# Kernel optimization log

Hardware: AMD Instinct MI355X
Metric: run time of the kernel (lower is better)

The kernel has to match this reference:

```python
import jax, jax.numpy as jnp
import numpy as np

BOX = 256      # box_size
OS = 1         # oversampling
NC = 10        # n_classes
B = 16         # batch
N = 262144     # points per example


def setup_inputs() -> dict:
    key = jax.random.key(0)
    k1, k2 = jax.random.split(key)
    # coordinates in [-0.5, 0.5) so (points+0.5)*S lies inside the grid
    points = jax.random.uniform(k1, (B, 2, N), dtype=jnp.float32, minval=-0.5, maxval=0.5)
    values = jax.random.normal(k2, (B, NC, N), dtype=jnp.float32)
    return {"points": points, "values": values}


def reference(points, values):
    S = BOX * OS
    b, nc = points.shape[0], values.shape[1]
    # [B,2,N] -> [B,N,2], scaled into pixel coords
    p = jnp.swapaxes((points + 0.5) * S, 1, 2)
    xyf = jnp.floor(p)
    r = p - xyf                       # fractional part, [B,N,2]
    xy = xyf.astype(jnp.int32)
    x, y = xy[..., 0], xy[..., 1]     # [B,N]
    rx, ry = r[..., 0], r[..., 1]

    im = jnp.zeros((b, nc, S * S), dtype=values.dtype)

    def scat(acc, idx, contrib):
        # acc [NC, S*S], idx [N], contrib [NC, N]
        return acc.at[:, idx].add(contrib)

    scat_b = jax.vmap(scat)  # over batch

    # 4-corner bilinear (CIC) deposition
    for dx in (0, 1):
        x_ = x + dx
        wx = (1 - dx) + (2 * dx - 1) * rx
        for dy in (0, 1):
            y_ = y + dy
            wy = (1 - dy) + (2 * dy - 1) * ry
            valid = (x_ >= 0) & (x_ < S) & (y_ >= 0) & (y_ < S)
            idx = jnp.where(valid, y_ * S + x_, 0)           # [B,N]
            w = jnp.where(valid, wx * wy, 0.0)               # [B,N]
            im = scat_b(im, idx, w[:, None, :] * values)     # [B,NC,S*S]

    return im.reshape(b, nc, S, S)
```

## Files before the change

### kernel.cpp

```cpp
#include <hip/hip_runtime.h>

#define S_     256
#define NC_    10
#define CHUNK  1024
#define NBIN   256
#define CAPR   1536
#define CAP    1536
#define RSTR   7

typedef unsigned int u32;

__device__ __forceinline__ u32 f2bf(float f) {
    u32 u = __float_as_uint(f);
    return (u + 0x7fffu + ((u >> 16) & 1u)) >> 16;
}
__device__ __forceinline__ float bf2f(u32 h) { return __uint_as_float(h << 16); }


__global__ void __launch_bounds__(256)
k_scatter(const float* __restrict__ points, const float* __restrict__ values,
          u32* __restrict__ cursor, u32* __restrict__ ovfCnt,
          u32* __restrict__ ovfBuf, uint2* __restrict__ recs, int N) {
    __shared__ u32 cnt[NBIN];
    __shared__ u32 gOff[NBIN];
    __shared__ u32 wsum[4];
    __shared__ unsigned char binId[CHUNK];
    __shared__ u32 lw[6][CHUNK];

    const int tid = threadIdx.x;
    const int cpb = N / CHUNK;
    const int b  = blockIdx.x / cpb;
    const int n0 = (blockIdx.x % cpb) * CHUNK;
    const float* pb = points + (size_t)b * 2 * N;
    const float* vb = values + (size_t)b * NC_ * N;
    const int nb = n0 + tid * 4;

    cnt[tid] = 0;

    const float4 pxv = *(const float4*)(pb + nb);
    const float4 pyv = *(const float4*)(pb + (size_t)N + nb);
    float4 vv[NC_];
#pragma unroll
    for (int c = 0; c < NC_; ++c)
        vv[c] = *(const float4*)(vb + (size_t)c * N + nb);

    __syncthreads();

    float px4[4] = {pxv.x, pxv.y, pxv.z, pxv.w};
    float py4[4] = {pyv.x, pyv.y, pyv.z, pyv.w};
    u32 w0[4], binA[4];
#pragma unroll
    for (int k = 0; k < 4; ++k) {
        float px = (px4[k] + 0.5f) * (float)S_;
        float py = (py4[k] + 0.5f) * (float)S_;
        int xi = (int)floorf(px), yi = (int)floorf(py);
        u32 qx = __float2uint_rn((px - (float)(xi & ~15)) * 2048.0f);
        u32 qy = __float2uint_rn((py - (float)(yi & ~15)) * 2048.0f);
        qx = min(qx, 32767u); qy = min(qy, 32767u);
        w0[k] = qx | (qy << 16);
        binA[k] = (u32)(((yi >> 4) << 4) + (xi >> 4));
        atomicAdd(&cnt[binA[k]], 1u);
    }
    __syncthreads();

    u32 myCnt = cnt[tid];
    u32 x = myCnt;
#pragma unroll
    for (int off = 1; off < 64; off <<= 1) {
        u32 y = __shfl_up(x, off, 64);
        if ((tid & 63) >= off) x += y;
    }
    if ((tid & 63) == 63) wsum[tid >> 6] = x;
    __syncthreads();
    u32 add = 0;
#pragma unroll
    for (int w = 0; w < 4; ++w) add += (w < (tid >> 6)) ? wsum[w] : 0;
    u32 excl = x - myCnt + add;

    const u32 gt = (u32)b * NBIN + (u32)tid;
    u32 gbase = 0;
    if (myCnt) gbase = gt * (u32)CAPR + atomicAdd(&cursor[gt], myCnt);
    gOff[tid] = gbase - excl;
    cnt[tid] = excl;
    __syncthreads();

#pragma unroll
    for (int k = 0; k < 4; ++k) {
        u32 bin = binA[k];
        u32 slot = atomicAdd(&cnt[bin], 1u);
        binId[slot] = (unsigned char)bin;
#define VG(c) ((&vv[c].x)[k])
        lw[0][slot] = w0[k];
        lw[1][slot] = f2bf(VG(0)) | (f2bf(VG(1)) << 16);
        lw[2][slot] = f2bf(VG(2)) | (f2bf(VG(3)) << 16);
        lw[3][slot] = f2bf(VG(4)) | (f2bf(VG(5)) << 16);
        lw[4][slot] = f2bf(VG(6)) | (f2bf(VG(7)) << 16);
        lw[5][slot] = f2bf(VG(8)) | (f2bf(VG(9)) << 16);
#undef VG
    }
    __syncthreads();

    const u32 tb0 = (u32)b * NBIN;
#pragma unroll
    for (int k = 0; k < 4; ++k) {
        u32 r = (u32)tid + (u32)k * 256;
        u32 bin = binId[r];
        u32 dst = gOff[bin] + r;
        u32 a0 = lw[0][r], a1 = lw[1][r], a2 = lw[2][r],
            a3 = lw[3][r], a4 = lw[4][r], a5 = lw[5][r];
        u32 rel = dst - (tb0 + bin) * (u32)CAPR;
        if (rel < (u32)CAPR) {
            size_t s3 = (size_t)dst * 3;
            recs[s3]     = make_uint2(a0, a1);
            recs[s3 + 1] = make_uint2(a2, a3);
            recs[s3 + 2] = make_uint2(a4, a5);
        } else {
            u32 oi = atomicAdd(ovfCnt, 1u);
            u32* ob = ovfBuf + (size_t)oi * 7;
            ob[0] = tb0 + bin;
            ob[1] = a0; ob[2] = a1; ob[3] = a2;
            ob[4] = a3; ob[5] = a4; ob[6] = a5;
        }
    }
}

__global__ void __launch_bounds__(256)
k_fused(const uint2* __restrict__ recs, const u32* __restrict__ cursor,
        float* __restrict__ out, float* __restrict__ borderBuf) {
    __shared__ u32 cnt[NBIN];
    __shared__ u32 excl[NBIN];
    __shared__ u32 wsum[4];
    __shared__ u32 lrec[CAP * RSTR];

    const int tid = threadIdx.x;
    const int g = blockIdx.x;
    const int batch = g >> 8, t = g & 255;
    const int ox = (t & 15) * 16, oy = (t >> 4) * 16;
    const u32 base = (u32)g * (u32)CAPR;
    const u32 n = min(cursor[g], (u32)CAP);

    cnt[tid] = 0;
    __syncthreads();

    u32 r[6][6];
    int cell[6];
#pragma unroll
    for (int k = 0; k < 6; ++k) {
        int i = k * 256 + tid;
        cell[k] = -1;
        if (i < (int)n) {
            size_t sa = (size_t)(base + i) * 3;
            uint2 a = recs[sa], b2 = recs[sa + 1], c2 = recs[sa + 2];
            r[k][0] = a.x;  r[k][1] = a.y;
            r[k][2] = b2.x; r[k][3] = b2.y;
            r[k][4] = c2.x; r[k][5] = c2.y;
            u32 qx = a.x & 0xffffu, qy = a.x >> 16;
            cell[k] = (int)(((qy >> 11) << 4) | (qx >> 11));
            atomicAdd(&cnt[cell[k]], 1u);
        }
    }
    __syncthreads();

    u32 c = cnt[tid];
    u32 x = c;
#pragma unroll
    for (int off = 1; off < 64; off <<= 1) {
        u32 y = __shfl_up(x, off, 64);
        if ((tid & 63) >= off) x += y;
    }
    if ((tid & 63) == 63) wsum[tid >> 6] = x;
    __syncthreads();
    u32 add = 0;
#pragma unroll
    for (int w = 0; w < 4; ++w) add += (w < (tid >> 6)) ? wsum[w] : 0;
    u32 ex = x - c + add;
    excl[tid] = ex;
    cnt[tid] = ex;
    __syncthreads();

#pragma unroll
    for (int k = 0; k < 6; ++k) {
        if (cell[k] >= 0) {
            u32 o = atomicAdd(&cnt[cell[k]], 1u) * RSTR;
#pragma unroll
            for (int w = 0; w < 6; ++w) lrec[o + w] = r[k][w];
        }
    }
    __syncthreads();

    for (int p = tid; p < 289; p += 256) {
        int lx = p % 17, ly = p / 17;
        float acc[NC_];
#pragma unroll
        for (int q = 0; q < NC_; ++q) acc[q] = 0.0f;
#pragma unroll
        for (int dy = 0; dy < 2; ++dy) {
            int cy = ly - 1 + dy;
            if ((unsigned)cy >= 16u) continue;
#pragma unroll
            for (int dx = 0; dx < 2; ++dx) {
                int cx = lx - 1 + dx;
                if ((unsigned)cx >= 16u) continue;
                int cc = (cy << 4) | cx;
                u32 j1 = cnt[cc];
                for (u32 j = excl[cc]; j < j1; ++j) {
                    u32 o = j * RSTR;
                    u32 w0 = lrec[o];
                    float rx = (float)(w0 & 2047u)         * (1.0f / 2048.0f);
                    float ry = (float)((w0 >> 16) & 2047u) * (1.0f / 2048.0f);
                    float w = (dx ? (1.0f - rx) : rx) * (dy ? (1.0f - ry) : ry);
                    u32 w1 = lrec[o + 1], w2 = lrec[o + 2], w3 = lrec[o + 3],
                        w4 = lrec[o + 4], w5 = lrec[o + 5];
                    acc[0] += w * bf2f(w1 & 0xffffu); acc[1] += w * bf2f(w1 >> 16);
                    acc[2] += w * bf2f(w2 & 0xffffu); acc[3] += w * bf2f(w2 >> 16);
                    acc[4] += w * bf2f(w3 & 0xffffu); acc[5] += w * bf2f(w3 >> 16);
                    acc[6] += w * bf2f(w4 & 0xffffu); acc[7] += w * bf2f(w4 >> 16);
                    acc[8] += w * bf2f(w5 & 0xffffu); acc[9] += w * bf2f(w5 >> 16);
                }
            }
        }
        bool interior = (lx >= 1) & (lx <= 15) & (ly >= 1) & (ly <= 15);
        if (interior) {
            int gx = ox + lx, gy = oy + ly;
            float* ob = out + (size_t)batch * NC_ * S_ * S_ + gy * S_ + gx;
#pragma unroll
            for (int q = 0; q < NC_; ++q) ob[(size_t)q * S_ * S_] = acc[q];
        } else {
            float* bb = borderBuf + ((size_t)g * 289 + p) * NC_;
#pragma unroll
            for (int q = 0; q < NC_; ++q) bb[q] = acc[q];
        }
    }
}

#define CLEAN_T 4096
__global__ void __launch_bounds__(256)
k_border(const float* __restrict__ borderBuf, float* __restrict__ out,
         const u32* __restrict__ ovfCnt, const u32* __restrict__ ovfBuf,
         int total) {
    int idx = blockIdx.x * 256 + threadIdx.x;
    if (idx >= total) {
        u32 oc = *ovfCnt;
        for (u32 j = (u32)(idx - total); j < oc; j += CLEAN_T) {
            const u32* ob = ovfBuf + (size_t)j * 7;
            u32 g = ob[0];
            int batch = (int)(g >> 8), t = (int)(g & 255u);
            int ox = (t & 15) * 16, oy = (t >> 4) * 16;
            u32 w0 = ob[1];
            u32 qx = w0 & 0xffffu, qy = w0 >> 16;
            int xi = ox + (int)(qx >> 11), yi = oy + (int)(qy >> 11);
            float rx = (float)(qx & 2047u) * (1.0f / 2048.0f);
            float ry = (float)(qy & 2047u) * (1.0f / 2048.0f);
            float v[NC_];
            v[0] = bf2f(ob[2] & 0xffffu); v[1] = bf2f(ob[2] >> 16);
            v[2] = bf2f(ob[3] & 0xffffu); v[3] = bf2f(ob[3] >> 16);
            v[4] = bf2f(ob[4] & 0xffffu); v[5] = bf2f(ob[4] >> 16);
            v[6] = bf2f(ob[5] & 0xffffu); v[7] = bf2f(ob[5] >> 16);
            v[8] = bf2f(ob[6] & 0xffffu); v[9] = bf2f(ob[6] >> 16);
            float* obase = out + (size_t)batch * NC_ * S_ * S_;
            for (int dx = 0; dx < 2; ++dx) {
                int x_ = xi + dx; if (x_ >= S_) continue;
                float wx = dx ? rx : (1.0f - rx);
                for (int dy = 0; dy < 2; ++dy) {
                    int y_ = yi + dy; if (y_ >= S_) continue;
                    float w = wx * (dy ? ry : (1.0f - ry));
                    for (int cc = 0; cc < NC_; ++cc)
                        atomicAdd(obase + (size_t)cc * S_ * S_ + y_ * S_ + x_,
                                  w * v[cc]);
                }
            }
        }
        return;
    }
    int b = idx / 7936;
    int j = idx - b * 7936;
    int gx, gy;
    if (j < 4096) {
        gx = (j >> 8) << 4;
        gy = j & 255;
    } else {
        int j2 = j - 4096;
        int row = j2 / 240, col = j2 - row * 240;
        gy = row << 4;
        gx = col + 1 + col / 15;
    }

    int txs[2], lxs[2], nx = 0;
    bool bx = (gx & 15) == 0, by = (gy & 15) == 0;
    if (bx) {
        if (gx > 0) { txs[nx] = (gx >> 4) - 1; lxs[nx] = 16; ++nx; }
        txs[nx] = gx >> 4; lxs[nx] = 0; ++nx;
    } else { txs[0] = gx >> 4; lxs[0] = gx & 15; nx = 1; }
    int tys[2], lys[2], ny = 0;
    if (by) {
        if (gy > 0) { tys[ny] = (gy >> 4) - 1; lys[ny] = 16; ++ny; }
        tys[ny] = gy >> 4; lys[ny] = 0; ++ny;
    } else { tys[0] = gy >> 4; lys[0] = gy & 15; ny = 1; }

    float acc[NC_];
#pragma unroll
    for (int q = 0; q < NC_; ++q) acc[q] = 0.0f;
    for (int jj = 0; jj < ny; ++jj)
        for (int ii = 0; ii < nx; ++ii) {
            int g = (b << 8) + (tys[jj] << 4) + txs[ii];
            int p = lys[jj] * 17 + lxs[ii];
            const float* bb = borderBuf + ((size_t)g * 289 + p) * NC_;
#pragma unroll
            for (int q = 0; q < NC_; ++q) acc[q] += bb[q];
        }
    float* ob = out + (size_t)b * NC_ * S_ * S_ + gy * S_ + gx;
#pragma unroll
    for (int q = 0; q < NC_; ++q) ob[(size_t)q * S_ * S_] = acc[q];
}

__global__ void __launch_bounds__(256)
scatter_cic_kernel(const float* __restrict__ points,
                   const float* __restrict__ values,
                   float* __restrict__ out, int N) {
    const int n = blockIdx.x * blockDim.x + threadIdx.x;
    const int b = blockIdx.y;
    if (n >= N) return;
    const float* pb = points + (size_t)b * 2 * N;
    const float px = (pb[n] + 0.5f) * (float)S_;
    const float py = (pb[(size_t)N + n] + 0.5f) * (float)S_;
    const float xf = floorf(px), yf = floorf(py);
    const float rx = px - xf, ry = py - yf;
    const int xi = (int)xf, yi = (int)yf;
    const float* vb = values + (size_t)b * NC_ * N + n;
    float v[NC_];
#pragma unroll
    for (int c = 0; c < NC_; ++c) v[c] = vb[(size_t)c * N];
    float* ob = out + (size_t)b * NC_ * S_ * S_;
#pragma unroll
    for (int dx = 0; dx < 2; ++dx) {
        const int x_ = xi + dx;
        if (x_ < 0 || x_ >= S_) continue;
        const float wx = dx ? rx : (1.0f - rx);
#pragma unroll
        for (int dy = 0; dy < 2; ++dy) {
            const int y_ = yi + dy;
            if (y_ < 0 || y_ >= S_) continue;
            const float w = wx * (dy ? ry : (1.0f - ry));
            const int idx = y_ * S_ + x_;
#pragma unroll
            for (int c = 0; c < NC_; ++c)
                atomicAdd(ob + (size_t)c * S_ * S_ + idx, w * v[c]);
        }
    }
}

extern "C" void kernel_launch(void* const* d_in, const int* in_sizes, int n_in,
                              void* d_out, int out_size, void* d_ws, size_t ws_size,
                              hipStream_t stream) {
    const float* points = (const float*)d_in[0];
    const float* values = (const float*)d_in[1];
    float* out = (float*)d_out;

    const int B = out_size / (NC_ * S_ * S_);
    const int N = in_sizes[0] / (2 * B);

    const size_t P = (size_t)B * N;
    const int cpb = N / CHUNK;
    const int chunksTotal = B * cpb;
    const int nTiles = B * NBIN;

    const size_t recBytes    = (size_t)nTiles * CAPR * 24;
    const size_t borderElems = (size_t)nTiles * 289 * NC_;
    const size_t ovfBytes    = P * 7 * 4;
    const size_t wsNeeded    = recBytes + (size_t)(nTiles + 1) * 4 +
                               borderElems * 4 + ovfBytes + 256;

    const bool fast = (N % CHUNK == 0) && (N >= CHUNK) && (B > 0) &&
                      (P < (1u << 31) / 2) && (ws_size >= wsNeeded);

    if (fast) {
        char* w = (char*)d_ws;
        uint2* recsA     = (uint2*)w;
        u32* cursor      = (u32*)(w + recBytes);
        u32* ovfCnt      = cursor + nTiles;
        float* borderBuf = (float*)(ovfCnt + 1);
        u32* ovfBuf      = (u32*)(borderBuf + borderElems);

        hipMemsetAsync(cursor, 0, (size_t)(nTiles + 1) * 4, stream);
        k_scatter<<<chunksTotal, 256, 0, stream>>>(points, values, cursor,
                                                   ovfCnt, ovfBuf, recsA, N);
        k_fused<<<nTiles, 256, 0, stream>>>(recsA, cursor, out, borderBuf);
        const int borderTotal = B * 7936;
        k_border<<<borderTotal / 256 + CLEAN_T / 256, 256, 0, stream>>>(
            borderBuf, out, ovfCnt, ovfBuf, borderTotal);
    } else {
        hipMemsetAsync(d_out, 0, (size_t)out_size * sizeof(float), stream);
        dim3 block(256, 1, 1);
        dim3 grid((N + 255) / 256, B, 1);
        scatter_cic_kernel<<<grid, block, 0, stream>>>(points, values, out, N);
    }
}
```

Measured before the change: 389.2 us.

## Switch to 32x32 tiles with LDS atomic image accumulation instead of cell-sorted gather

```diff
diff --git a/kernel.cpp b/kernel.cpp
--- a/kernel.cpp
+++ b/kernel.cpp
@@ -3,10 +3,11 @@
 #define S_     256
 #define NC_    10
 #define CHUNK  1024
-#define NBIN   256
-#define CAPR   1536
-#define CAP    1536
-#define RSTR   7
+#define TS     32
+#define NBIN2  64
+#define CAPR   4608
+#define IW     33
+#define IMSZ   (NC_ * IW * IW)
 
 typedef unsigned int u32;
 
@@ -21,9 +22,8 @@
 k_scatter(const float* __restrict__ points, const float* __restrict__ values,
           u32* __restrict__ cursor, u32* __restrict__ ovfCnt,
           u32* __restrict__ ovfBuf, uint2* __restrict__ recs, int N) {
-    __shared__ u32 cnt[NBIN];
-    __shared__ u32 gOff[NBIN];
-    __shared__ u32 wsum[4];
+    __shared__ u32 cnt[NBIN2];
+    __shared__ u32 gOff[NBIN2];
     __shared__ unsigned char binId[CHUNK];
     __shared__ u32 lw[6][CHUNK];
 
@@ -35,7 +35,7 @@
     const float* vb = values + (size_t)b * NC_ * N;
     const int nb = n0 + tid * 4;
 
-    cnt[tid] = 0;
+    if (tid < NBIN2) cnt[tid] = 0;
 
     const float4 pxv = *(const float4*)(pb + nb);
     const float4 pyv = *(const float4*)(pb + (size_t)N + nb);
@@ -54,34 +54,30 @@
         float px = (px4[k] + 0.5f) * (float)S_;
         float py = (py4[k] + 0.5f) * (float)S_;
         int xi = (int)floorf(px), yi = (int)floorf(py);
-        u32 qx = __float2uint_rn((px - (float)(xi & ~15)) * 2048.0f);
-        u32 qy = __float2uint_rn((py - (float)(yi & ~15)) * 2048.0f);
-        qx = min(qx, 32767u); qy = min(qy, 32767u);
+        u32 qx = __float2uint_rn((px - (float)(xi & ~31)) * 2048.0f);
+        u32 qy = __float2uint_rn((py - (float)(yi & ~31)) * 2048.0f);
+        qx = min(qx, 65535u); qy = min(qy, 65535u);
         w0[k] = qx | (qy << 16);
-        binA[k] = (u32)(((yi >> 4) << 4) + (xi >> 4));
+        binA[k] = (u32)(((yi >> 5) << 3) + (xi >> 5));
         atomicAdd(&cnt[binA[k]], 1u);
     }
     __syncthreads();
 
-    u32 myCnt = cnt[tid];
-    u32 x = myCnt;
-#pragma unroll
-    for (int off = 1; off < 64; off <<= 1) {
-        u32 y = __shfl_up(x, off, 64);
-        if ((tid & 63) >= off) x += y;
-    }
-    if ((tid & 63) == 63) wsum[tid >> 6] = x;
-    __syncthreads();
-    u32 add = 0;
-#pragma unroll
-    for (int w = 0; w < 4; ++w) add += (w < (tid >> 6)) ? wsum[w] : 0;
-    u32 excl = x - myCnt + add;
-
-    const u32 gt = (u32)b * NBIN + (u32)tid;
-    u32 gbase = 0;
-    if (myCnt) gbase = gt * (u32)CAPR + atomicAdd(&cursor[gt], myCnt);
-    gOff[tid] = gbase - excl;
-    cnt[tid] = excl;
+    if (tid < NBIN2) {
+        u32 myCnt = cnt[tid];
+        u32 x = myCnt;
+#pragma unroll
+        for (int off = 1; off < 64; off <<= 1) {
+            u32 y = __shfl_up(x, off, 64);
+            if (tid >= off) x += y;
+        }
+        u32 excl = x - myCnt;
+        u32 gt = (u32)b * NBIN2 + (u32)tid;
+        u32 gbase = 0;
+        if (myCnt) gbase = gt * (u32)CAPR + atomicAdd(&cursor[gt], myCnt);
+        gOff[tid] = gbase - excl;
+        cnt[tid] = excl;
+    }
     __syncthreads();
 
 #pragma unroll
@@ -100,7 +96,7 @@
     }
     __syncthreads();
 
-    const u32 tb0 = (u32)b * NBIN;
+    const u32 tb0 = (u32)b * NBIN2;
 #pragma unroll
     for (int k = 0; k < 4; ++k) {
         u32 r = (u32)tid + (u32)k * 256;
@@ -127,108 +123,61 @@
 __global__ void __launch_bounds__(256)
 k_fused(const uint2* __restrict__ recs, const u32* __restrict__ cursor,
         float* __restrict__ out, float* __restrict__ borderBuf) {
-    __shared__ u32 cnt[NBIN];
-    __shared__ u32 excl[NBIN];
-    __shared__ u32 wsum[4];
-    __shared__ u32 lrec[CAP * RSTR];
+    __shared__ float img[IMSZ];
 
     const int tid = threadIdx.x;
     const int g = blockIdx.x;
-    const int batch = g >> 8, t = g & 255;
-    const int ox = (t & 15) * 16, oy = (t >> 4) * 16;
+    const int batch = g >> 6, t = g & 63;
+    const int ox = (t & 7) * TS, oy = (t >> 3) * TS;
     const u32 base = (u32)g * (u32)CAPR;
-    const u32 n = min(cursor[g], (u32)CAP);
-
-    cnt[tid] = 0;
-    __syncthreads();
-
-    u32 r[6][6];
-    int cell[6];
-#pragma unroll
-    for (int k = 0; k < 6; ++k) {
-        int i = k * 256 + tid;
-        cell[k] = -1;
-        if (i < (int)n) {
-            size_t sa = (size_t)(base + i) * 3;
-            uint2 a = recs[sa], b2 = recs[sa + 1], c2 = recs[sa + 2];
-            r[k][0] = a.x;  r[k][1] = a.y;
-            r[k][2] = b2.x; r[k][3] = b2.y;
-            r[k][4] = c2.x; r[k][5] = c2.y;
-            u32 qx = a.x & 0xffffu, qy = a.x >> 16;
-            cell[k] = (int)(((qy >> 11) << 4) | (qx >> 11));
-            atomicAdd(&cnt[cell[k]], 1u);
-        }
-    }
-    __syncthreads();
-
-    u32 c = cnt[tid];
-    u32 x = c;
-#pragma unroll
-    for (int off = 1; off < 64; off <<= 1) {
-        u32 y = __shfl_up(x, off, 64);
-        if ((tid & 63) >= off) x += y;
-    }
-    if ((tid & 63) == 63) wsum[tid >> 6] = x;
-    __syncthreads();
-    u32 add = 0;
-#pragma unroll
-    for (int w = 0; w < 4; ++w) add += (w < (tid >> 6)) ? wsum[w] : 0;
-    u32 ex = x - c + add;
-    excl[tid] = ex;
-    cnt[tid] = ex;
-    __syncthreads();
-
-#pragma unroll
-    for (int k = 0; k < 6; ++k) {
-        if (cell[k] >= 0) {
-            u32 o = atomicAdd(&cnt[cell[k]], 1u) * RSTR;
-#pragma unroll
-            for (int w = 0; w < 6; ++w) lrec[o + w] = r[k][w];
-        }
-    }
-    __syncthreads();
-
-    for (int p = tid; p < 289; p += 256) {
-        int lx = p % 17, ly = p / 17;
-        float acc[NC_];
-#pragma unroll
-        for (int q = 0; q < NC_; ++q) acc[q] = 0.0f;
-#pragma unroll
-        for (int dy = 0; dy < 2; ++dy) {
-            int cy = ly - 1 + dy;
-            if ((unsigned)cy >= 16u) continue;
-#pragma unroll
-            for (int dx = 0; dx < 2; ++dx) {
-                int cx = lx - 1 + dx;
-                if ((unsigned)cx >= 16u) continue;
-                int cc = (cy << 4) | cx;
-                u32 j1 = cnt[cc];
-                for (u32 j = excl[cc]; j < j1; ++j) {
-                    u32 o = j * RSTR;
-                    u32 w0 = lrec[o];
-                    float rx = (float)(w0 & 2047u)         * (1.0f / 2048.0f);
-                    float ry = (float)((w0 >> 16) & 2047u) * (1.0f / 2048.0f);
-                    float w = (dx ? (1.0f - rx) : rx) * (dy ? (1.0f - ry) : ry);
-                    u32 w1 = lrec[o + 1], w2 = lrec[o + 2], w3 = lrec[o + 3],
-                        w4 = lrec[o + 4], w5 = lrec[o + 5];
-                    acc[0] += w * bf2f(w1 & 0xffffu); acc[1] += w * bf2f(w1 >> 16);
-                    acc[2] += w * bf2f(w2 & 0xffffu); acc[3] += w * bf2f(w2 >> 16);
-                    acc[4] += w * bf2f(w3 & 0xffffu); acc[5] += w * bf2f(w3 >> 16);
-                    acc[6] += w * bf2f(w4 & 0xffffu); acc[7] += w * bf2f(w4 >> 16);
-                    acc[8] += w * bf2f(w5 & 0xffffu); acc[9] += w * bf2f(w5 >> 16);
-                }
-            }
-        }
-        bool interior = (lx >= 1) & (lx <= 15) & (ly >= 1) & (ly <= 15);
+    const u32 n = min(cursor[g], (u32)CAPR);
+
+    for (int p = tid; p < IMSZ; p += 256) img[p] = 0.0f;
+    __syncthreads();
+
+    for (u32 i = tid; i < n; i += 256) {
+        size_t sa = (size_t)(base + i) * 3;
+        uint2 a = recs[sa], b2 = recs[sa + 1], c2 = recs[sa + 2];
+        u32 qx = a.x & 0xffffu, qy = a.x >> 16;
+        int xi = (int)(qx >> 11), yi = (int)(qy >> 11);
+        float rx = (float)(qx & 2047u) * (1.0f / 2048.0f);
+        float ry = (float)(qy & 2047u) * (1.0f / 2048.0f);
+        float w00 = (1.0f - rx) * (1.0f - ry);
+        float w10 = rx * (1.0f - ry);
+        float w01 = (1.0f - rx) * ry;
+        float w11 = rx * ry;
+        int p00 = yi * IW + xi;
+        float v[NC_];
+        v[0] = bf2f(a.y & 0xffffu);  v[1] = bf2f(a.y >> 16);
+        v[2] = bf2f(b2.x & 0xffffu); v[3] = bf2f(b2.x >> 16);
+        v[4] = bf2f(b2.y & 0xffffu); v[5] = bf2f(b2.y >> 16);
+        v[6] = bf2f(c2.x & 0xffffu); v[7] = bf2f(c2.x >> 16);
+        v[8] = bf2f(c2.y & 0xffffu); v[9] = bf2f(c2.y >> 16);
+#pragma unroll
+        for (int c = 0; c < NC_; ++c) {
+            float vc = v[c];
+            float* ib = img + c * (IW * IW) + p00;
+            atomicAdd(ib,          w00 * vc);
+            atomicAdd(ib + 1,      w10 * vc);
+            atomicAdd(ib + IW,     w01 * vc);
+            atomicAdd(ib + IW + 1, w11 * vc);
+        }
+    }
+    __syncthreads();
+
+    for (int p = tid; p < IW * IW; p += 256) {
+        int lx = p % IW, ly = p / IW;
+        bool interior = (lx >= 1) & (lx <= 31) & (ly >= 1) & (ly <= 31);
         if (interior) {
             int gx = ox + lx, gy = oy + ly;
             float* ob = out + (size_t)batch * NC_ * S_ * S_ + gy * S_ + gx;
 #pragma unroll
-            for (int q = 0; q < NC_; ++q) ob[(size_t)q * S_ * S_] = acc[q];
+            for (int q = 0; q < NC_; ++q)
+                ob[(size_t)q * S_ * S_] = img[q * (IW * IW) + p];
         } else {
-            float* bb = borderBuf + ((size_t)g * 289 + p) * NC_;
-#pragma unroll
-            for (int q = 0; q < NC_; ++q) bb[q] = acc[q];
+            float* bb = borderBuf + ((size_t)g * (IW * IW) + p) * NC_;
+#pragma unroll
+            for (int q = 0; q < NC_; ++q) bb[q] = img[q * (IW * IW) + p];
         }
     }
 }
@@ -244,8 +193,8 @@
         for (u32 j = (u32)(idx - total); j < oc; j += CLEAN_T) {
             const u32* ob = ovfBuf + (size_t)j * 7;
             u32 g = ob[0];
-            int batch = (int)(g >> 8), t = (int)(g & 255u);
-            int ox = (t & 15) * 16, oy = (t >> 4) * 16;
+            int batch = (int)(g >> 6), t = (int)(g & 63u);
+            int ox = (t & 7) * TS, oy = (t >> 3) * TS;
             u32 w0 = ob[1];
             u32 qx = w0 & 0xffffu, qy = w0 >> 16;
             int xi = ox + (int)(qx >> 11), yi = oy + (int)(qy >> 11);
@@ -272,39 +221,39 @@
         }
         return;
     }
-    int b = idx / 7936;
-    int j = idx - b * 7936;
+    int b = idx / 4032;
+    int j = idx - b * 4032;
     int gx, gy;
-    if (j < 4096) {
-        gx = (j >> 8) << 4;
+    if (j < 2048) {
+        gx = (j >> 8) << 5;
         gy = j & 255;
     } else {
-        int j2 = j - 4096;
-        int row = j2 / 240, col = j2 - row * 240;
-        gy = row << 4;
-        gx = col + 1 + col / 15;
+        int j2 = j - 2048;
+        int row = j2 / 248, col = j2 - row * 248;
+        gy = row << 5;
+        gx = col + 1 + col / 31;
     }
 
     int txs[2], lxs[2], nx = 0;
-    bool bx = (gx & 15) == 0, by = (gy & 15) == 0;
+    bool bx = (gx & 31) == 0, by = (gy & 31) == 0;
     if (bx) {
-        if (gx > 0) { txs[nx] = (gx >> 4) - 1; lxs[nx] = 16; ++nx; }
-        txs[nx] = gx >> 4; lxs[nx] = 0; ++nx;
-    } else { txs[0] = gx >> 4; lxs[0] = gx & 15; nx = 1; }
+        if (gx > 0) { txs[nx] = (gx >> 5) - 1; lxs[nx] = 32; ++nx; }
+        txs[nx] = gx >> 5; lxs[nx] = 0; ++nx;
+    } else { txs[0] = gx >> 5; lxs[0] = gx & 31; nx = 1; }
     int tys[2], lys[2], ny = 0;
     if (by) {
-        if (gy > 0) { tys[ny] = (gy >> 4) - 1; lys[ny] = 16; ++ny; }
-        tys[ny] = gy >> 4; lys[ny] = 0; ++ny;
-    } else { tys[0] = gy >> 4; lys[0] = gy & 15; ny = 1; }
+        if (gy > 0) { tys[ny] = (gy >> 5) - 1; lys[ny] = 32; ++ny; }
+        tys[ny] = gy >> 5; lys[ny] = 0; ++ny;
+    } else { tys[0] = gy >> 5; lys[0] = gy & 31; ny = 1; }
 
     float acc[NC_];
 #pragma unroll
     for (int q = 0; q < NC_; ++q) acc[q] = 0.0f;
     for (int jj = 0; jj < ny; ++jj)
         for (int ii = 0; ii < nx; ++ii) {
-            int g = (b << 8) + (tys[jj] << 4) + txs[ii];
-            int p = lys[jj] * 17 + lxs[ii];
-            const float* bb = borderBuf + ((size_t)g * 289 + p) * NC_;
+            int g = (b << 6) + (tys[jj] << 3) + txs[ii];
+            int p = lys[jj] * IW + lxs[ii];
+            const float* bb = borderBuf + ((size_t)g * (IW * IW) + p) * NC_;
 #pragma unroll
             for (int q = 0; q < NC_; ++q) acc[q] += bb[q];
         }
@@ -362,12 +311,12 @@
     const size_t P = (size_t)B * N;
     const int cpb = N / CHUNK;
     const int chunksTotal = B * cpb;
-    const int nTiles = B * NBIN;
-
-    const size_t recBytes    = (size_t)nTiles * CAPR * 24;
-    const size_t borderElems = (size_t)nTiles * 289 * NC_;
+    const int nSlab = B * NBIN2;
+
+    const size_t recBytes    = (size_t)nSlab * CAPR * 24;
+    const size_t borderElems = (size_t)nSlab * (IW * IW) * NC_;
     const size_t ovfBytes    = P * 7 * 4;
-    const size_t wsNeeded    = recBytes + (size_t)(nTiles + 1) * 4 +
+    const size_t wsNeeded    = recBytes + (size_t)(nSlab + 1) * 4 +
                                borderElems * 4 + ovfBytes + 256;
 
     const bool fast = (N % CHUNK == 0) && (N >= CHUNK) && (B > 0) &&
@@ -377,16 +326,16 @@
         char* w = (char*)d_ws;
         uint2* recsA     = (uint2*)w;
         u32* cursor      = (u32*)(w + recBytes);
-        u32* ovfCnt      = cursor + nTiles;
+        u32* ovfCnt      = cursor + nSlab;
         float* borderBuf = (float*)(ovfCnt + 1);
         u32* ovfBuf      = (u32*)(borderBuf + borderElems);
 
-        hipMemsetAsync(cursor, 0, (size_t)(nTiles + 1) * 4, stream);
+        hipMemsetAsync(cursor, 0, (size_t)(nSlab + 1) * 4, stream);
         k_scatter<<<chunksTotal, 256, 0, stream>>>(points, values, cursor,
                                                    ovfCnt, ovfBuf, recsA, N);
-        k_fused<<<nTiles, 256, 0, stream>>>(recsA, cursor, out, borderBuf);
-        const int borderTotal = B * 7936;
-        k_border<<<borderTotal / 256 + CLEAN_T / 256, 256, 0, stream>>>(
+        k_fused<<<nSlab, 256, 0, stream>>>(recsA, cursor, out, borderBuf);
+        const int borderTotal = B * 4032;
+        k_border<<<(borderTotal + 255) / 256 + CLEAN_T / 256, 256, 0, stream>>>(
             borderBuf, out, ovfCnt, ovfBuf, borderTotal);
     } else {
         hipMemsetAsync(d_out, 0, (size_t)out_size * sizeof(float), stream);
```

Measured after the change: 1.135 ms. 2.92x slower.
